# Performance work log

Measured on AMD Instinct MI355X. Metric: run time of the kernel, lower is better.

The kernel has to match this reference:

```python
import jax, jax.numpy as jnp
import numpy as np

N_NODES = 100000
N_EDGES = 1600000
IN_DIM = 128
HID = 128


def sage_conv(x, src, dst, W_l, W_r, b, num_nodes):
    # PyG SAGEConv (mean aggregation): out = lin_l(mean_{j in N(i)} x_j) + lin_r(x_i)
    msgs = x[src]                                            # [E, F] gather
    agg = jax.ops.segment_sum(msgs, dst, num_segments=num_nodes)  # [N, F]
    cnt = jax.ops.segment_sum(jnp.ones((src.shape[0],), x.dtype), dst,
                              num_segments=num_nodes)        # [N]
    agg = agg / jnp.maximum(cnt, 1.0)[:, None]               # mean; 0 for isolated nodes
    return agg @ W_l + b + x @ W_r


def setup_inputs() -> dict:
    key = jax.random.key(0)
    ks = jax.random.split(key, 12)
    s_in = 1.0 / np.sqrt(IN_DIM)
    s_h = 1.0 / np.sqrt(HID)
    return {
        "x": jax.random.normal(ks[0], (N_NODES, IN_DIM), jnp.float32),
        "edge_index": jax.random.randint(ks[1], (2, N_EDGES), 0, N_NODES, jnp.int64),
        "Wl1": jax.random.normal(ks[2], (IN_DIM, HID), jnp.float32) * s_in,
        "Wr1": jax.random.normal(ks[3], (IN_DIM, HID), jnp.float32) * s_in,
        "b1": jnp.zeros((HID,), jnp.float32),
        "Wl2": jax.random.normal(ks[4], (HID, HID), jnp.float32) * s_h,
        "Wr2": jax.random.normal(ks[5], (HID, HID), jnp.float32) * s_h,
        "b2": jnp.zeros((HID,), jnp.float32),
        "Wp": jax.random.normal(ks[6], (HID, 1), jnp.float32) * s_h,
        "bp": jnp.zeros((1,), jnp.float32),
        "Wd": jax.random.normal(ks[7], (HID, 1), jnp.float32) * s_h,
        "bd": jnp.zeros((1,), jnp.float32),
    }


def reference(x, edge_index, Wl1, Wr1, b1, Wl2, Wr2, b2, Wp, bp, Wd, bd):
    src, dst = edge_index[0], edge_index[1]
    h = jax.nn.relu(sage_conv(x, src, dst, Wl1, Wr1, b1, N_NODES))
    h = jax.nn.relu(sage_conv(h, src, dst, Wl2, Wr2, b2, N_NODES))
    preds = h @ Wp + bp                      # [N, 1]
    diffs = jax.nn.sigmoid(h @ Wd + bd)      # [N, 1]
    return (preds - diffs, preds + diffs)
```

## Files before the change

kernel.cpp:

```cpp
#include <hip/hip_runtime.h>
#include <hip/hip_bf16.h>

#define N_NODES 100000
#define N_EDGES 1600000
#define NBUCK 1563
#define BCAP 1216
#define PADC 1408
#define ACHUNK 4096
#define GTILES 1563

typedef __bf16 bf16x8 __attribute__((ext_vector_type(8)));
typedef __bf16 bf16x4 __attribute__((ext_vector_type(4)));
typedef float  f32x4  __attribute__((ext_vector_type(4)));
typedef float  f32x2  __attribute__((ext_vector_type(2)));



__global__ __launch_bounds__(256) void init_kernel(int* __restrict__ bcnt,
                                                   int* __restrict__ P1s,
                                                   int* __restrict__ P2s,
                                                   const float* __restrict__ Wl1,
                                                   const float* __restrict__ Wr1,
                                                   const float* __restrict__ Wl2,
                                                   const float* __restrict__ Wr2,
                                                   __bf16* __restrict__ W1out,
                                                   __bf16* __restrict__ W2out) {
  const int b = blockIdx.x, t = threadIdx.x;
  if (b == 0) {
    for (int i = t; i < NBUCK; i += 256) bcnt[i] = 0;
    if (t < 32) { P1s[t] = 0; P2s[t] = 0; }
    return;
  }
  int gi = (b - 1) * 256 + t;
  bool L2 = gi >= 32768;
  int i = gi & 32767;
  int j = i & 7;
  int lane = (i >> 3) & 63;
  int c = (i >> 9) & 3;
  int tile = i >> 11;
  int k = c * 32 + ((lane >> 4) * 8) + j;
  int krow = L2 ? (((k & 7) << 4) | (k >> 3)) : k;
  int col = tile * 16 + (lane & 15);
  const float* Wl = L2 ? Wl2 : Wl1;
  const float* Wr = L2 ? Wr2 : Wr1;
  float v = (col < 128) ? Wl[krow * 128 + col] : Wr[krow * 128 + (col - 128)];
  (L2 ? W2out : W1out)[i] = (__bf16)v;
}


__global__ __launch_bounds__(256, 2) void work1_kernel(
    const float* __restrict__ A, const __bf16* __restrict__ Wswz,
    const float* __restrict__ bias, unsigned char* __restrict__ P,
    __bf16* __restrict__ R, int M,
    const int* __restrict__ src, const int* __restrict__ dst,
    int* __restrict__ bcnt, unsigned* __restrict__ packed, int E) {
  __shared__ __align__(16) char smem[64 * 144 * 2];
  const int t = threadIdx.x;

  if (blockIdx.x >= GTILES) {
    int* hist = (int*)smem;
    int* curs = (int*)(smem + 6272);
    for (int i = t; i < NBUCK; i += 256) hist[i] = 0;
    __syncthreads();

    const int base = (blockIdx.x - GTILES) * ACHUNK;
    const int lim = min(base + ACHUNK, E);

    int dloc[16], sloc[16];
    int myn = 0;
    for (int i = base + t; i < lim; i += 256) {
      dloc[myn] = dst[i];
      sloc[myn] = src[i];
      ++myn;
    }
    for (int k = 0; k < myn; ++k) atomicAdd(&hist[dloc[k] >> 6], 1);
    __syncthreads();

    for (int i = t; i < NBUCK; i += 256) {
      int h = hist[i];
      curs[i] = (h > 0) ? atomicAdd(&bcnt[i], h) : 0;
    }
    __syncthreads();

    for (int k = 0; k < myn; ++k) {
      int d = dloc[k];
      int b = d >> 6;
      int pos = atomicAdd(&curs[b], 1);
      if (pos < BCAP)
        packed[(size_t)b * BCAP + pos] = ((unsigned)sloc[k] << 6) | (unsigned)(d & 63);
    }
    return;
  }

  __bf16 (*ldsA)[144] = (__bf16 (*)[144])smem;
  const int lane = t & 63;
  const int w = t >> 6;
  const int q = lane >> 4;
  const int s = lane & 15;
  const int m0 = blockIdx.x * 64;

  bf16x8 bfrag[16];
#pragma unroll
  for (int ct = 0; ct < 4; ++ct)
#pragma unroll
    for (int c = 0; c < 4; ++c)
      bfrag[ct * 4 + c] =
          *(const bf16x8*)&Wswz[(size_t)((((w * 4 + ct) * 4 + c) * 64) + lane) * 8];

#pragma unroll
  for (int it = 0; it < 8; ++it) {
    int row = it * 8 + (t >> 5);
    int col = (t & 31) * 4;
    float4 v = make_float4(0.f, 0.f, 0.f, 0.f);
    if (m0 + row < M) v = *(const float4*)&A[(size_t)(m0 + row) * 128 + col];
    bf16x4 bv;
    bv.x = (__bf16)v.x; bv.y = (__bf16)v.y; bv.z = (__bf16)v.z; bv.w = (__bf16)v.w;
    *(bf16x4*)&ldsA[row][col] = bv;
  }

  float breg[4];
#pragma unroll
  for (int j = 0; j < 4; ++j)
    breg[j] = (w >= 2) ? bias[((w - 2) * 4 + j) * 16 + s] : 0.f;

  __syncthreads();

  bf16x8 afrag[16];
#pragma unroll
  for (int rt = 0; rt < 4; ++rt)
#pragma unroll
    for (int c = 0; c < 4; ++c)
      afrag[rt * 4 + c] = *(const bf16x8*)&ldsA[rt * 16 + s][c * 32 + q * 8];

  f32x4 acc[16];
  f32x4 zero = {0.f, 0.f, 0.f, 0.f};
#pragma unroll
  for (int i = 0; i < 16; ++i) acc[i] = zero;

#pragma unroll
  for (int c = 0; c < 4; ++c)
#pragma unroll
    for (int rt = 0; rt < 4; ++rt)
#pragma unroll
      for (int ct = 0; ct < 4; ++ct)
        acc[rt * 4 + ct] = __builtin_amdgcn_mfma_f32_16x16x32_bf16(
            afrag[rt * 4 + c], bfrag[ct * 4 + c], acc[rt * 4 + ct], 0, 0, 0);

#pragma unroll
  for (int rt = 0; rt < 4; ++rt) {
#pragma unroll
    for (int r = 0; r < 4; ++r) {
      int row = m0 + rt * 16 + q * 4 + r;
      if (row < M) {
        if (w < 2) {
          unsigned v = 0;
          v = __builtin_amdgcn_cvt_pk_fp8_f32(acc[rt * 4 + 0][r], acc[rt * 4 + 1][r], v, false);
          v = __builtin_amdgcn_cvt_pk_fp8_f32(acc[rt * 4 + 2][r], acc[rt * 4 + 3][r], v, true);
          *(unsigned*)&P[(size_t)row * 128 + s * 8 + w * 4] = v;
        } else {
          bf16x4 o;
#pragma unroll
          for (int ct = 0; ct < 4; ++ct) o[ct] = (__bf16)(acc[rt * 4 + ct][r] + breg[ct]);
          *(bf16x4*)&R[(size_t)row * 128 + s * 8 + (w - 2) * 4] = o;
        }
      }
    }
  }
}



__global__ __launch_bounds__(256, 2) void fusedB_kernel(
    const unsigned char* __restrict__ P1, __bf16* R,
    const unsigned* __restrict__ pck, const int* __restrict__ bcnt,
    const __bf16* __restrict__ Wswz, const float* __restrict__ bias,
    unsigned char* __restrict__ P2, int N) {
  __shared__ __bf16 Hlds[64][144];
  __shared__ int ssrcL[PADC];
  __shared__ int hist[64], pexcl[64], curs[64], scanb[64];
  __shared__ int gsteal;
  const int t = threadIdx.x;
  const int lane = t & 63;
  const int w = t >> 6;
  const int q = lane >> 4;
  const int s = lane & 15;
  const int b = blockIdx.x, nb = b * 64;

  bf16x8 bfrag[16];
#pragma unroll
  for (int ct = 0; ct < 4; ++ct)
#pragma unroll
    for (int c = 0; c < 4; ++c)
      bfrag[ct * 4 + c] =
          *(const bf16x8*)&Wswz[(size_t)((((w * 4 + ct) * 4 + c) * 64) + lane) * 8];

  float breg[4];
#pragma unroll
  for (int j = 0; j < 4; ++j)
    breg[j] = (w >= 2) ? bias[((w - 2) * 4 + j) * 16 + s] : 0.f;

  if (t < 64) hist[t] = 0;
  if (t == 0) gsteal = 0;
  __syncthreads();

  const int ecnt = min(bcnt[b], BCAP);
  const unsigned* pk = pck + (size_t)b * BCAP;
  unsigned ploc[5];
  int myn = 0;
  for (int i = t; i < ecnt; i += 256) {
    unsigned p = pk[i];
    ploc[myn++] = p;
    atomicAdd(&hist[p & 63u], 1);
  }
  __syncthreads();

  int c0 = (t < 64) ? hist[t] : 0;
  int pc = (c0 + 3) & ~3;
  int x = pc;
  if (t < 64) scanb[t] = x;
  __syncthreads();
  for (int d = 1; d < 64; d <<= 1) {
    int y = (t >= d && t < 64) ? scanb[t - d] : 0;
    __syncthreads();
    if (t < 64) { x += y; scanb[t] = x; }
    __syncthreads();
  }
  if (t < 64) { pexcl[t] = x - pc; curs[t] = x - pc; }
  __syncthreads();

  for (int k = 0; k < myn; ++k) {
    unsigned p = ploc[k];
    int r = atomicAdd(&curs[p & 63u], 1);
    ssrcL[r] = (int)(p >> 6);
  }
  if (t < 64)
    for (int j = c0; j < pc; ++j) ssrcL[pexcl[t] + j] = N;
  __syncthreads();

  const unsigned char* Pb = P1 + (size_t)s * 8;
  for (;;) {
    int n4;
    if (lane == 0) n4 = atomicAdd(&gsteal, 4);
    n4 = __shfl(n4, 0, 64);
    if (n4 >= 64) break;
    int dl = n4 + q;
    int node = nb + dl;
    int start = pexcl[dl];
    int dg = hist[dl];
    int pend = start + ((dg + 3) & ~3);

    f32x2 a01 = {0.f, 0.f}, a23 = {0.f, 0.f}, a45 = {0.f, 0.f}, a67 = {0.f, 0.f};
    for (int cur = start; cur < pend; cur += 4) {
      int4 sv = *(const int4*)&ssrcL[cur];
      uint2 v0 = *(const uint2*)(Pb + (size_t)sv.x * 128);
      uint2 v1 = *(const uint2*)(Pb + (size_t)sv.y * 128);
      uint2 v2 = *(const uint2*)(Pb + (size_t)sv.z * 128);
      uint2 v3 = *(const uint2*)(Pb + (size_t)sv.w * 128);
      a01 += __builtin_amdgcn_cvt_pk_f32_fp8(v0.x, false);
      a23 += __builtin_amdgcn_cvt_pk_f32_fp8(v0.x, true);
      a45 += __builtin_amdgcn_cvt_pk_f32_fp8(v0.y, false);
      a67 += __builtin_amdgcn_cvt_pk_f32_fp8(v0.y, true);
      a01 += __builtin_amdgcn_cvt_pk_f32_fp8(v1.x, false);
      a23 += __builtin_amdgcn_cvt_pk_f32_fp8(v1.x, true);
      a45 += __builtin_amdgcn_cvt_pk_f32_fp8(v1.y, false);
      a67 += __builtin_amdgcn_cvt_pk_f32_fp8(v1.y, true);
      a01 += __builtin_amdgcn_cvt_pk_f32_fp8(v2.x, false);
      a23 += __builtin_amdgcn_cvt_pk_f32_fp8(v2.x, true);
      a45 += __builtin_amdgcn_cvt_pk_f32_fp8(v2.y, false);
      a67 += __builtin_amdgcn_cvt_pk_f32_fp8(v2.y, true);
      a01 += __builtin_amdgcn_cvt_pk_f32_fp8(v3.x, false);
      a23 += __builtin_amdgcn_cvt_pk_f32_fp8(v3.x, true);
      a45 += __builtin_amdgcn_cvt_pk_f32_fp8(v3.y, false);
      a67 += __builtin_amdgcn_cvt_pk_f32_fp8(v3.y, true);
    }

    int nc = min(node, N - 1);
    float inv = 1.0f / (float)(dg > 0 ? dg : 1);
    bf16x8 rv = *(const bf16x8*)&R[(size_t)nc * 128 + s * 8];
    float acc1[8] = {a01[0], a01[1], a23[0], a23[1], a45[0], a45[1], a67[0], a67[1]};
    bf16x8 hh;
#pragma unroll
    for (int j = 0; j < 8; ++j)
      hh[j] = (__bf16)fmaxf(acc1[j] * inv + (float)rv[j], 0.f);
    *(bf16x8*)&Hlds[dl][s * 8] = hh;
  }
  __syncthreads();

  bf16x8 afrag[16];
#pragma unroll
  for (int rt = 0; rt < 4; ++rt)
#pragma unroll
    for (int c = 0; c < 4; ++c)
      afrag[rt * 4 + c] = *(const bf16x8*)&Hlds[rt * 16 + s][c * 32 + q * 8];

  f32x4 acc[16];
  f32x4 zero = {0.f, 0.f, 0.f, 0.f};
#pragma unroll
  for (int i = 0; i < 16; ++i) acc[i] = zero;

#pragma unroll
  for (int c = 0; c < 4; ++c)
#pragma unroll
    for (int rt = 0; rt < 4; ++rt)
#pragma unroll
      for (int ct = 0; ct < 4; ++ct)
        acc[rt * 4 + ct] = __builtin_amdgcn_mfma_f32_16x16x32_bf16(
            afrag[rt * 4 + c], bfrag[ct * 4 + c], acc[rt * 4 + ct], 0, 0, 0);

#pragma unroll
  for (int rt = 0; rt < 4; ++rt) {
#pragma unroll
    for (int r = 0; r < 4; ++r) {
      int row = nb + rt * 16 + q * 4 + r;
      if (row < N) {
        if (w < 2) {
          unsigned v = 0;
          v = __builtin_amdgcn_cvt_pk_fp8_f32(acc[rt * 4 + 0][r], acc[rt * 4 + 1][r], v, false);
          v = __builtin_amdgcn_cvt_pk_fp8_f32(acc[rt * 4 + 2][r], acc[rt * 4 + 3][r], v, true);
          *(unsigned*)&P2[(size_t)row * 128 + s * 8 + w * 4] = v;
        } else {
          bf16x4 o;
#pragma unroll
          for (int ct = 0; ct < 4; ++ct) o[ct] = (__bf16)(acc[rt * 4 + ct][r] + breg[ct]);
          *(bf16x4*)&R[(size_t)row * 128 + s * 8 + (w - 2) * 4] = o;
        }
      }
    }
  }
}


__global__ __launch_bounds__(256) void fusedC_kernel(
    const unsigned char* __restrict__ P2, const __bf16* __restrict__ R,
    const unsigned* __restrict__ pck, const int* __restrict__ bcnt,
    float* __restrict__ out,
    const float* __restrict__ Wp, const float* __restrict__ Wd,
    const float* __restrict__ bp, const float* __restrict__ bd, int N) {
  __shared__ int ssrcL[PADC];
  __shared__ int hist[64], pexcl[64], curs[64], scanb[64];
  __shared__ int gsteal;
  const int t = threadIdx.x;
  const int lane = t & 63;
  const int q = lane >> 4;
  const int s = lane & 15;
  const int b = blockIdx.x, nb = b * 64;

  if (t < 64) hist[t] = 0;
  if (t == 0) gsteal = 0;
  __syncthreads();

  const int ecnt = min(bcnt[b], BCAP);
  const unsigned* pk = pck + (size_t)b * BCAP;
  unsigned ploc[5];
  int myn = 0;
  for (int i = t; i < ecnt; i += 256) {
    unsigned p = pk[i];
    ploc[myn++] = p;
    atomicAdd(&hist[p & 63u], 1);
  }
  __syncthreads();

  int c0 = (t < 64) ? hist[t] : 0;
  int pc = (c0 + 3) & ~3;
  int x = pc;
  if (t < 64) scanb[t] = x;
  __syncthreads();
  for (int d = 1; d < 64; d <<= 1) {
    int y = (t >= d && t < 64) ? scanb[t - d] : 0;
    __syncthreads();
    if (t < 64) { x += y; scanb[t] = x; }
    __syncthreads();
  }
  if (t < 64) { pexcl[t] = x - pc; curs[t] = x - pc; }
  __syncthreads();

  for (int k = 0; k < myn; ++k) {
    unsigned p = ploc[k];
    int r = atomicAdd(&curs[p & 63u], 1);
    ssrcL[r] = (int)(p >> 6);
  }
  if (t < 64)
    for (int j = c0; j < pc; ++j) ssrcL[pexcl[t] + j] = N;
  __syncthreads();

  const unsigned char* Pb = P2 + (size_t)s * 8;
  for (;;) {
    int n4;
    if (lane == 0) n4 = atomicAdd(&gsteal, 4);
    n4 = __shfl(n4, 0, 64);
    if (n4 >= 64) break;
    int dl = n4 + q;
    int node = nb + dl;
    int start = pexcl[dl];
    int dg = hist[dl];
    int pend = start + ((dg + 3) & ~3);

    f32x2 a01 = {0.f, 0.f}, a23 = {0.f, 0.f}, a45 = {0.f, 0.f}, a67 = {0.f, 0.f};
    for (int cur = start; cur < pend; cur += 4) {
      int4 sv = *(const int4*)&ssrcL[cur];
      uint2 v0 = *(const uint2*)(Pb + (size_t)sv.x * 128);
      uint2 v1 = *(const uint2*)(Pb + (size_t)sv.y * 128);
      uint2 v2 = *(const uint2*)(Pb + (size_t)sv.z * 128);
      uint2 v3 = *(const uint2*)(Pb + (size_t)sv.w * 128);
      a01 += __builtin_amdgcn_cvt_pk_f32_fp8(v0.x, false);
      a23 += __builtin_amdgcn_cvt_pk_f32_fp8(v0.x, true);
      a45 += __builtin_amdgcn_cvt_pk_f32_fp8(v0.y, false);
      a67 += __builtin_amdgcn_cvt_pk_f32_fp8(v0.y, true);
      a01 += __builtin_amdgcn_cvt_pk_f32_fp8(v1.x, false);
      a23 += __builtin_amdgcn_cvt_pk_f32_fp8(v1.x, true);
      a45 += __builtin_amdgcn_cvt_pk_f32_fp8(v1.y, false);
      a67 += __builtin_amdgcn_cvt_pk_f32_fp8(v1.y, true);
      a01 += __builtin_amdgcn_cvt_pk_f32_fp8(v2.x, false);
      a23 += __builtin_amdgcn_cvt_pk_f32_fp8(v2.x, true);
      a45 += __builtin_amdgcn_cvt_pk_f32_fp8(v2.y, false);
      a67 += __builtin_amdgcn_cvt_pk_f32_fp8(v2.y, true);
      a01 += __builtin_amdgcn_cvt_pk_f32_fp8(v3.x, false);
      a23 += __builtin_amdgcn_cvt_pk_f32_fp8(v3.x, true);
      a45 += __builtin_amdgcn_cvt_pk_f32_fp8(v3.y, false);
      a67 += __builtin_amdgcn_cvt_pk_f32_fp8(v3.y, true);
    }

    int nc = min(node, N - 1);
    float inv = 1.0f / (float)(dg > 0 ? dg : 1);
    bf16x8 rv = *(const bf16x8*)&R[(size_t)nc * 128 + s * 8];
    float acc[8] = {a01[0], a01[1], a23[0], a23[1], a45[0], a45[1], a67[0], a67[1]};
    float p = 0.f, dd = 0.f;
#pragma unroll
    for (int j = 0; j < 8; ++j) {
      float h = fmaxf(acc[j] * inv + (float)rv[j], 0.f);
      p += h * Wp[j * 16 + s];
      dd += h * Wd[j * 16 + s];
    }
    p += __shfl_xor(p, 1, 64);  p += __shfl_xor(p, 2, 64);
    p += __shfl_xor(p, 4, 64);  p += __shfl_xor(p, 8, 64);
    dd += __shfl_xor(dd, 1, 64); dd += __shfl_xor(dd, 2, 64);
    dd += __shfl_xor(dd, 4, 64); dd += __shfl_xor(dd, 8, 64);
    if (node < N && s == 0) {
      float preds = p + bp[0];
      float sg = 1.0f / (1.0f + __expf(-(dd + bd[0])));
      out[node] = preds - sg;
      out[N + node] = preds + sg;
    }
  }
}


extern "C" void kernel_launch(void* const* d_in, const int* in_sizes, int n_in,
                              void* d_out, int out_size, void* d_ws, size_t ws_size,
                              hipStream_t stream) {
  const float* x    = (const float*)d_in[0];
  const int*   ei   = (const int*)d_in[1];
  const float* Wl1 = (const float*)d_in[2];
  const float* Wr1 = (const float*)d_in[3];
  const float* b1  = (const float*)d_in[4];
  const float* Wl2 = (const float*)d_in[5];
  const float* Wr2 = (const float*)d_in[6];
  const float* b2  = (const float*)d_in[7];
  const float* Wp  = (const float*)d_in[8];
  const float* bp  = (const float*)d_in[9];
  const float* Wd  = (const float*)d_in[10];
  const float* bd  = (const float*)d_in[11];
  float* out = (float*)d_out;

  const int N = N_NODES, E = N_EDGES;
  const int* src = ei;
  const int* dst = ei + E;

  char* w = (char*)d_ws;
  unsigned char* P1 = (unsigned char*)w; w += (size_t)(N + 1) * 128;
  unsigned char* P2 = (unsigned char*)w; w += (size_t)(N + 1) * 128;
  __bf16* Rbuf   = (__bf16*)w;   w += (size_t)N * 128 * 2;
  unsigned* pck  = (unsigned*)w; w += (size_t)NBUCK * BCAP * 4;
  int* bcnt      = (int*)w;      w += (size_t)(NBUCK + 32) * 4;
  __bf16* Ws1    = (__bf16*)w;   w += 65536;
  __bf16* Ws2    = (__bf16*)w;   w += 65536;

  const int PABLK = (E + ACHUNK - 1) / ACHUNK;

  init_kernel<<<257, 256, 0, stream>>>(bcnt,
                                       (int*)(P1 + (size_t)N * 128),
                                       (int*)(P2 + (size_t)N * 128),
                                       Wl1, Wr1, Wl2, Wr2, Ws1, Ws2);
  work1_kernel<<<GTILES + PABLK, 256, 0, stream>>>(x, Ws1, b1, P1, Rbuf, N,
                                                   src, dst, bcnt, pck, E);
  fusedB_kernel<<<NBUCK, 256, 0, stream>>>(P1, Rbuf, pck, bcnt, Ws2, b2, P2, N);
  fusedC_kernel<<<NBUCK, 256, 0, stream>>>(P2, Rbuf, pck, bcnt, out,
                                           Wp, Wd, bp, bd, N);
}
```

Measured before the change: 248.3 us.

## Split GEMM epilogue into column halves to cut registers and raise occupancy

Both work1 and fusedB no longer hold all 16 B fragments, 16 A fragments and 16 accumulators in registers. The GEMM now runs in two column halves with 8 accumulators each, reloading A fragments from LDS and B fragments from global per k-chunk. Launch bounds go from 2 to 4 blocks per SM to raise occupancy and hide the latency of the gather and memory phases. In exchange, A fragments are read from LDS twice, B is loaded in the inner loop, and output stores are narrower (2-byte fp8 pairs and bf16x2 instead of 4-wide writes).

```diff
diff --git a/kernel.cpp b/kernel.cpp
--- a/kernel.cpp
+++ b/kernel.cpp
@@ -11,6 +11,7 @@
 
 typedef __bf16 bf16x8 __attribute__((ext_vector_type(8)));
 typedef __bf16 bf16x4 __attribute__((ext_vector_type(4)));
+typedef __bf16 bf16x2 __attribute__((ext_vector_type(2)));
 typedef float  f32x4  __attribute__((ext_vector_type(4)));
 typedef float  f32x2  __attribute__((ext_vector_type(2)));
 
@@ -48,7 +49,7 @@
 }
 
 
-__global__ __launch_bounds__(256, 2) void work1_kernel(
+__global__ __launch_bounds__(256, 4) void work1_kernel(
     const float* __restrict__ A, const __bf16* __restrict__ Wswz,
     const float* __restrict__ bias, unsigned char* __restrict__ P,
     __bf16* __restrict__ R, int M,
@@ -98,14 +99,6 @@
   const int q = lane >> 4;
   const int s = lane & 15;
   const int m0 = blockIdx.x * 64;
-
-  bf16x8 bfrag[16];
-#pragma unroll
-  for (int ct = 0; ct < 4; ++ct)
-#pragma unroll
-    for (int c = 0; c < 4; ++c)
-      bfrag[ct * 4 + c] =
-          *(const bf16x8*)&Wswz[(size_t)((((w * 4 + ct) * 4 + c) * 64) + lane) * 8];
 
 #pragma unroll
   for (int it = 0; it < 8; ++it) {
@@ -117,60 +110,61 @@
     bv.x = (__bf16)v.x; bv.y = (__bf16)v.y; bv.z = (__bf16)v.z; bv.w = (__bf16)v.w;
     *(bf16x4*)&ldsA[row][col] = bv;
   }
-
-  float breg[4];
-#pragma unroll
-  for (int j = 0; j < 4; ++j)
-    breg[j] = (w >= 2) ? bias[((w - 2) * 4 + j) * 16 + s] : 0.f;
-
-  __syncthreads();
-
-  bf16x8 afrag[16];
-#pragma unroll
-  for (int rt = 0; rt < 4; ++rt)
-#pragma unroll
-    for (int c = 0; c < 4; ++c)
-      afrag[rt * 4 + c] = *(const bf16x8*)&ldsA[rt * 16 + s][c * 32 + q * 8];
-
-  f32x4 acc[16];
-  f32x4 zero = {0.f, 0.f, 0.f, 0.f};
-#pragma unroll
-  for (int i = 0; i < 16; ++i) acc[i] = zero;
-
-#pragma unroll
-  for (int c = 0; c < 4; ++c)
-#pragma unroll
-    for (int rt = 0; rt < 4; ++rt)
-#pragma unroll
-      for (int ct = 0; ct < 4; ++ct)
-        acc[rt * 4 + ct] = __builtin_amdgcn_mfma_f32_16x16x32_bf16(
-            afrag[rt * 4 + c], bfrag[ct * 4 + c], acc[rt * 4 + ct], 0, 0, 0);
-
-#pragma unroll
-  for (int rt = 0; rt < 4; ++rt) {
-#pragma unroll
-    for (int r = 0; r < 4; ++r) {
-      int row = m0 + rt * 16 + q * 4 + r;
-      if (row < M) {
-        if (w < 2) {
-          unsigned v = 0;
-          v = __builtin_amdgcn_cvt_pk_fp8_f32(acc[rt * 4 + 0][r], acc[rt * 4 + 1][r], v, false);
-          v = __builtin_amdgcn_cvt_pk_fp8_f32(acc[rt * 4 + 2][r], acc[rt * 4 + 3][r], v, true);
-          *(unsigned*)&P[(size_t)row * 128 + s * 8 + w * 4] = v;
-        } else {
-          bf16x4 o;
-#pragma unroll
-          for (int ct = 0; ct < 4; ++ct) o[ct] = (__bf16)(acc[rt * 4 + ct][r] + breg[ct]);
-          *(bf16x4*)&R[(size_t)row * 128 + s * 8 + (w - 2) * 4] = o;
+  __syncthreads();
+
+#pragma unroll
+  for (int half = 0; half < 2; ++half) {
+    f32x4 acc[8];
+    f32x4 zero = {0.f, 0.f, 0.f, 0.f};
+#pragma unroll
+    for (int i = 0; i < 8; ++i) acc[i] = zero;
+
+#pragma unroll
+    for (int c = 0; c < 4; ++c) {
+      bf16x8 b0 = *(const bf16x8*)&Wswz[(size_t)((((w * 4 + half * 2 + 0) * 4 + c) * 64) + lane) * 8];
+      bf16x8 b1 = *(const bf16x8*)&Wswz[(size_t)((((w * 4 + half * 2 + 1) * 4 + c) * 64) + lane) * 8];
+#pragma unroll
+      for (int rt = 0; rt < 4; ++rt) {
+        bf16x8 a = *(const bf16x8*)&ldsA[rt * 16 + s][c * 32 + q * 8];
+        acc[rt * 2 + 0] = __builtin_amdgcn_mfma_f32_16x16x32_bf16(a, b0, acc[rt * 2 + 0], 0, 0, 0);
+        acc[rt * 2 + 1] = __builtin_amdgcn_mfma_f32_16x16x32_bf16(a, b1, acc[rt * 2 + 1], 0, 0, 0);
+      }
+    }
+
+    if (w < 2) {
+#pragma unroll
+      for (int rt = 0; rt < 4; ++rt) {
+#pragma unroll
+        for (int r = 0; r < 4; ++r) {
+          int row = m0 + rt * 16 + q * 4 + r;
+          if (row < M) {
+            unsigned v = __builtin_amdgcn_cvt_pk_fp8_f32(acc[rt * 2 + 0][r], acc[rt * 2 + 1][r], 0, false);
+            *(unsigned short*)&P[(size_t)row * 128 + s * 8 + w * 4 + half * 2] = (unsigned short)v;
+          }
         }
       }
+    } else {
+      float b0v = bias[((w - 2) * 4 + half * 2 + 0) * 16 + s];
+      float b1v = bias[((w - 2) * 4 + half * 2 + 1) * 16 + s];
+#pragma unroll
+      for (int rt = 0; rt < 4; ++rt) {
+#pragma unroll
+        for (int r = 0; r < 4; ++r) {
+          int row = m0 + rt * 16 + q * 4 + r;
+          if (row < M) {
+            bf16x2 o;
+            o[0] = (__bf16)(acc[rt * 2 + 0][r] + b0v);
+            o[1] = (__bf16)(acc[rt * 2 + 1][r] + b1v);
+            *(bf16x2*)&R[(size_t)row * 128 + s * 8 + (w - 2) * 4 + half * 2] = o;
+          }
+        }
+      }
     }
   }
 }
 
 
-
-__global__ __launch_bounds__(256, 2) void fusedB_kernel(
+__global__ __launch_bounds__(256, 4) void fusedB_kernel(
     const unsigned char* __restrict__ P1, __bf16* R,
     const unsigned* __restrict__ pck, const int* __restrict__ bcnt,
     const __bf16* __restrict__ Wswz, const float* __restrict__ bias,
@@ -185,19 +179,6 @@
   const int q = lane >> 4;
   const int s = lane & 15;
   const int b = blockIdx.x, nb = b * 64;
-
-  bf16x8 bfrag[16];
-#pragma unroll
-  for (int ct = 0; ct < 4; ++ct)
-#pragma unroll
-    for (int c = 0; c < 4; ++c)
-      bfrag[ct * 4 + c] =
-          *(const bf16x8*)&Wswz[(size_t)((((w * 4 + ct) * 4 + c) * 64) + lane) * 8];
-
-  float breg[4];
-#pragma unroll
-  for (int j = 0; j < 4; ++j)
-    breg[j] = (w >= 2) ? bias[((w - 2) * 4 + j) * 16 + s] : 0.f;
 
   if (t < 64) hist[t] = 0;
   if (t == 0) gsteal = 0;
@@ -286,43 +267,51 @@
   }
   __syncthreads();
 
-  bf16x8 afrag[16];
-#pragma unroll
-  for (int rt = 0; rt < 4; ++rt)
-#pragma unroll
-    for (int c = 0; c < 4; ++c)
-      afrag[rt * 4 + c] = *(const bf16x8*)&Hlds[rt * 16 + s][c * 32 + q * 8];
-
-  f32x4 acc[16];
-  f32x4 zero = {0.f, 0.f, 0.f, 0.f};
-#pragma unroll
-  for (int i = 0; i < 16; ++i) acc[i] = zero;
-
-#pragma unroll
-  for (int c = 0; c < 4; ++c)
-#pragma unroll
-    for (int rt = 0; rt < 4; ++rt)
-#pragma unroll
-      for (int ct = 0; ct < 4; ++ct)
-        acc[rt * 4 + ct] = __builtin_amdgcn_mfma_f32_16x16x32_bf16(
-            afrag[rt * 4 + c], bfrag[ct * 4 + c], acc[rt * 4 + ct], 0, 0, 0);
-
-#pragma unroll
-  for (int rt = 0; rt < 4; ++rt) {
-#pragma unroll
-    for (int r = 0; r < 4; ++r) {
-      int row = nb + rt * 16 + q * 4 + r;
-      if (row < N) {
-        if (w < 2) {
-          unsigned v = 0;
-          v = __builtin_amdgcn_cvt_pk_fp8_f32(acc[rt * 4 + 0][r], acc[rt * 4 + 1][r], v, false);
-          v = __builtin_amdgcn_cvt_pk_fp8_f32(acc[rt * 4 + 2][r], acc[rt * 4 + 3][r], v, true);
-          *(unsigned*)&P2[(size_t)row * 128 + s * 8 + w * 4] = v;
-        } else {
-          bf16x4 o;
-#pragma unroll
-          for (int ct = 0; ct < 4; ++ct) o[ct] = (__bf16)(acc[rt * 4 + ct][r] + breg[ct]);
-          *(bf16x4*)&R[(size_t)row * 128 + s * 8 + (w - 2) * 4] = o;
+#pragma unroll
+  for (int half = 0; half < 2; ++half) {
+    f32x4 acc[8];
+    f32x4 zero = {0.f, 0.f, 0.f, 0.f};
+#pragma unroll
+    for (int i = 0; i < 8; ++i) acc[i] = zero;
+
+#pragma unroll
+    for (int c = 0; c < 4; ++c) {
+      bf16x8 b0 = *(const bf16x8*)&Wswz[(size_t)((((w * 4 + half * 2 + 0) * 4 + c) * 64) + lane) * 8];
+      bf16x8 b1 = *(const bf16x8*)&Wswz[(size_t)((((w * 4 + half * 2 + 1) * 4 + c) * 64) + lane) * 8];
+#pragma unroll
+      for (int rt = 0; rt < 4; ++rt) {
+        bf16x8 a = *(const bf16x8*)&Hlds[rt * 16 + s][c * 32 + q * 8];
+        acc[rt * 2 + 0] = __builtin_amdgcn_mfma_f32_16x16x32_bf16(a, b0, acc[rt * 2 + 0], 0, 0, 0);
+        acc[rt * 2 + 1] = __builtin_amdgcn_mfma_f32_16x16x32_bf16(a, b1, acc[rt * 2 + 1], 0, 0, 0);
+      }
+    }
+
+    if (w < 2) {
+#pragma unroll
+      for (int rt = 0; rt < 4; ++rt) {
+#pragma unroll
+        for (int r = 0; r < 4; ++r) {
+          int row = nb + rt * 16 + q * 4 + r;
+          if (row < N) {
+            unsigned v = __builtin_amdgcn_cvt_pk_fp8_f32(acc[rt * 2 + 0][r], acc[rt * 2 + 1][r], 0, false);
+            *(unsigned short*)&P2[(size_t)row * 128 + s * 8 + w * 4 + half * 2] = (unsigned short)v;
+          }
+        }
+      }
+    } else {
+      float b0v = bias[((w - 2) * 4 + half * 2 + 0) * 16 + s];
+      float b1v = bias[((w - 2) * 4 + half * 2 + 1) * 16 + s];
+#pragma unroll
+      for (int rt = 0; rt < 4; ++rt) {
+#pragma unroll
+        for (int r = 0; r < 4; ++r) {
+          int row = nb + rt * 16 + q * 4 + r;
+          if (row < N) {
+            bf16x2 o;
+            o[0] = (__bf16)(acc[rt * 2 + 0][r] + b0v);
+            o[1] = (__bf16)(acc[rt * 2 + 1][r] + b1v);
+            *(bf16x2*)&R[(size_t)row * 128 + s * 8 + (w - 2) * 4 + half * 2] = o;
+          }
         }
       }
     }
```

Result: no change. 249.2 us (+0.4%).
